# Kernel optimization log

Hardware: AMD Instinct MI355X
Metric: run time of the kernel (lower is better)

Reference implementation:

```python
import jax, jax.numpy as jnp
import numpy as np

BS, SEQ, ML, DEPTH = 32, 50, 16, 4
NN = 2 ** DEPTH - 1          # 15 nodes per complete binary tree (heap layout)
VOCAB, EMB, ENC = 50000, 128, 128
GH = 32                      # bigru hidden per direction
NC = 100                     # num_concepts
LH = 128                     # LSTM hidden
LIN = 2 + 2 * GH + NC + 1    # 167 LSTM feature dim


def _gru_dir(x, Wx, Wh, bx, bh, reverse):
    # x: [B, T, I]; torch GRU gate order r,z,n
    B, H = x.shape[0], Wh.shape[1]
    xe = jnp.einsum('bti,gi->btg', x, Wx) + bx   # [B,T,3H]
    xs = jnp.swapaxes(xe, 0, 1)
    if reverse:
        xs = xs[::-1]
    def step(h, xt):
        gh = h @ Wh.T + bh
        r = jax.nn.sigmoid(xt[:, :H] + gh[:, :H])
        z = jax.nn.sigmoid(xt[:, H:2 * H] + gh[:, H:2 * H])
        n = jnp.tanh(xt[:, 2 * H:] + r * gh[:, 2 * H:])
        hn = (1.0 - z) * n + z * h
        return hn, hn
    _, hs = jax.lax.scan(step, jnp.zeros((B, H), x.dtype), xs)
    if reverse:
        hs = hs[::-1]
    return jnp.swapaxes(hs, 0, 1)


def _lstm(x, Wx, Wh, bx, bh):
    # x: [B, T, I]; torch LSTM gate order i,f,g,o
    B, H = x.shape[0], Wh.shape[1]
    xe = jnp.einsum('bti,gi->btg', x, Wx) + bx   # [B,T,4H]
    def step(carry, xt):
        h, c = carry
        g = xt + h @ Wh.T + bh
        i = jax.nn.sigmoid(g[:, :H])
        f = jax.nn.sigmoid(g[:, H:2 * H])
        gg = jnp.tanh(g[:, 2 * H:3 * H])
        o = jax.nn.sigmoid(g[:, 3 * H:])
        c = f * c + i * gg
        h = o * jnp.tanh(c)
        return (h, c), h
    h0 = (jnp.zeros((B, H), x.dtype), jnp.zeros((B, H), x.dtype))
    _, hs = jax.lax.scan(step, h0, jnp.swapaxes(xe, 0, 1))
    return jnp.swapaxes(hs, 0, 1)


def setup_inputs() -> dict:
    key = jax.random.key(0)
    ks = jax.random.split(key, 24)
    p = {}
    p['p_id'] = jax.random.randint(ks[0], (BS, SEQ), 0, 1000)
    p['c_id'] = jax.random.randint(ks[1], (BS, SEQ), 0, NC)
    p['ast_tokens'] = jax.random.randint(ks[2], (BS, SEQ, ML, NN), 0, VOCAB)
    p['target_c'] = jax.nn.one_hot(jax.random.randint(ks[3], (BS, SEQ), 0, NC + 1), NC + 1, dtype=jnp.float32)
    p['c_embed'] = jax.random.normal(ks[4], (BS, SEQ, NC + 1), jnp.float32)
    p['cur_result'] = jax.random.normal(ks[5], (BS, SEQ, 2), jnp.float32)
    p['result'] = (jax.random.uniform(ks[6], (BS * SEQ,)) < 0.5).astype(jnp.float32)
    p['emb'] = jax.random.normal(ks[7], (VOCAB, EMB), jnp.float32) * 0.02
    p['Wc_w'] = jax.random.normal(ks[8], (ENC, EMB), jnp.float32) / np.sqrt(EMB)
    p['Wc_b'] = jnp.zeros((ENC,), jnp.float32)
    p['gru_WxF'] = jax.random.normal(ks[9], (3 * GH, ENC), jnp.float32) / np.sqrt(ENC)
    p['gru_WhF'] = jax.random.normal(ks[10], (3 * GH, GH), jnp.float32) / np.sqrt(GH)
    p['gru_bxF'] = jnp.zeros((3 * GH,), jnp.float32)
    p['gru_bhF'] = jnp.zeros((3 * GH,), jnp.float32)
    p['gru_WxB'] = jax.random.normal(ks[11], (3 * GH, ENC), jnp.float32) / np.sqrt(ENC)
    p['gru_WhB'] = jax.random.normal(ks[12], (3 * GH, GH), jnp.float32) / np.sqrt(GH)
    p['gru_bxB'] = jnp.zeros((3 * GH,), jnp.float32)
    p['gru_bhB'] = jnp.zeros((3 * GH,), jnp.float32)
    p['lstm_Wx'] = jax.random.normal(ks[13], (4 * LH, LIN), jnp.float32) / np.sqrt(LIN)
    p['lstm_Wh'] = jax.random.normal(ks[14], (4 * LH, LH), jnp.float32) / np.sqrt(LH)
    p['lstm_bx'] = jnp.zeros((4 * LH,), jnp.float32)
    p['lstm_bh'] = jnp.zeros((4 * LH,), jnp.float32)
    p['pred_w'] = jax.random.normal(ks[15], (NC + 1, LH), jnp.float32) / np.sqrt(LH)
    p['pred_b'] = jnp.zeros((NC + 1,), jnp.float32)
    return p


def reference(p_id, c_id, ast_tokens, target_c, c_embed, cur_result, result,
              emb, Wc_w, Wc_b,
              gru_WxF, gru_WhF, gru_bxF, gru_bhF,
              gru_WxB, gru_WhB, gru_bxB, gru_bhB,
              lstm_Wx, lstm_Wh, lstm_bx, lstm_bh,
              pred_w, pred_b):
    # BatchTreeEncoder: per-node W_c(emb(tok)), subtree-sum via bottom-up heap, max over nodes
    e = emb[ast_tokens] @ Wc_w.T + Wc_b          # [BS,SEQ,ML,NN,ENC]
    s = e
    for lvl in range(DEPTH - 2, -1, -1):          # bottom-up over fixed tree levels
        par = np.arange(2 ** lvl - 1, 2 ** (lvl + 1) - 1)
        s = s.at[..., par, :].add(s[..., 2 * par + 1, :] + s[..., 2 * par + 2, :])
    tree_enc = jnp.max(s, axis=3)                 # [BS,SEQ,ML,ENC]
    x = tree_enc.reshape(BS * SEQ, ML, ENC)
    hf = _gru_dir(x, gru_WxF, gru_WhF, gru_bxF, gru_bhF, False)
    hb = _gru_dir(x, gru_WxB, gru_WhB, gru_bxB, gru_bhB, True)
    gout = jnp.concatenate([hf, hb], axis=-1)     # [BS*SEQ, ML, 64]
    code = jnp.max(gout, axis=1).reshape(BS, SEQ, 2 * GH)  # max_pool1d over time
    lin = jnp.concatenate([c_embed, code, cur_result], axis=-1)  # [BS,SEQ,LIN]
    lout = _lstm(lin, lstm_Wx, lstm_Wh, lstm_bx, lstm_bh)         # [BS,SEQ,LH]
    pred = lout.reshape(BS * SEQ, LH) @ pred_w.T + pred_b         # [BS*SEQ, NC+1]
    tc = target_c.reshape(BS * SEQ, NC + 1)
    p1 = jnp.sum(pred * tc, axis=-1)              # bmm(pred, target_c)
    ncon = jnp.sum(tc, axis=-1)
    m = (ncon > 0).astype(pred.dtype)
    fp = p1 / jnp.maximum(ncon, 1.0)
    bce = jnp.maximum(fp, 0.0) - fp * result + jnp.log1p(jnp.exp(-jnp.abs(fp)))
    loss = jnp.sum(bce * m) / jnp.maximum(jnp.sum(m), 1.0)
    return loss, jax.nn.sigmoid(fp) * m, result * m
```

## Files before the change

kernel.cpp:

```cpp
#include <hip/hip_runtime.h>
#include <hip/hip_bf16.h>
#include <math.h>

#define BS 32
#define SEQ 50
#define ML 16
#define NN 15
#define NTREE (BS*SEQ*ML)
#define NROW (BS*SEQ)
#define VOCAB 50000
#define EMB 128
#define ENC 128
#define GH 32
#define NC 100
#define LH 128
#define LIN_D 167

typedef float f32x4 __attribute__((ext_vector_type(4)));
typedef short s16x8 __attribute__((ext_vector_type(8)));
typedef unsigned int u32;
typedef u32 u32x4v __attribute__((ext_vector_type(4)));

#define LOG2E 1.4426950408889634f
__device__ __forceinline__ float fsig(float x) {
  return __builtin_amdgcn_rcpf(1.f + __builtin_amdgcn_exp2f(-LOG2E * x));
}
__device__ __forceinline__ float ftanh(float x) {
  return 2.f * __builtin_amdgcn_rcpf(
             1.f + __builtin_amdgcn_exp2f(-2.f * LOG2E * x)) - 1.f;
}
__device__ __forceinline__ u32 pkbf(float x, float y) {
  u32 a = __float_as_uint(x), b = __float_as_uint(y);
  a = (a + 0x7FFFu + ((a >> 16) & 1u)) >> 16;
  b = (b + 0x7FFFu + ((b >> 16) & 1u)) >> 16;
  return a | (b << 16);
}
__device__ __forceinline__ unsigned short f2bf(float x) {
  u32 a = __float_as_uint(x);
  return (unsigned short)((a + 0x7FFFu + ((a >> 16) & 1u)) >> 16);
}
#define MFMA __builtin_amdgcn_mfma_f32_16x16x32_bf16

__global__ __launch_bounds__(256) void gemm_mfma(
    const float* __restrict__ A, const u32* __restrict__ Bpk,
    const float* __restrict__ bias, void* __restrict__ Cout,
    int M, int N, int out_bf16) {
  int w = threadIdx.x >> 6, lane = threadIdx.x & 63;
  int R0 = blockIdx.x * 64 + w * 16;
  int r = R0 + (lane & 15);
  int rm = (r < M) ? r : (M - 1);
  const float* Ar = A + (size_t)rm * 128 + (lane >> 4) * 8;
  s16x8 a0, a1, a2, a3;
  {
#define LDA(AF, KT) { \
    float4 f0 = *(const float4*)(Ar + KT * 32); \
    float4 f1 = *(const float4*)(Ar + KT * 32 + 4); \
    u32x4v q = {pkbf(f0.x, f0.y), pkbf(f0.z, f0.w), \
                pkbf(f1.x, f1.y), pkbf(f1.z, f1.w)}; \
    AF = __builtin_bit_cast(s16x8, q); }
    LDA(a0, 0) LDA(a1, 1) LDA(a2, 2) LDA(a3, 3)
#undef LDA
  }
  const u32x4v* Bp = (const u32x4v*)Bpk;
  for (int c = 0; c < N; c += 64) {
    f32x4 acc0, acc1, acc2, acc3;
    {
      float b0 = bias ? bias[c + (lane & 15)]      : 0.f;
      float b1 = bias ? bias[c + 16 + (lane & 15)] : 0.f;
      float b2 = bias ? bias[c + 32 + (lane & 15)] : 0.f;
      float b3 = bias ? bias[c + 48 + (lane & 15)] : 0.f;
      acc0 = (f32x4){b0, b0, b0, b0}; acc1 = (f32x4){b1, b1, b1, b1};
      acc2 = (f32x4){b2, b2, b2, b2}; acc3 = (f32x4){b3, b3, b3, b3};
    }
    int fbase = (c >> 4) * 4;
#define DONT(ACC, NT) { \
    s16x8 bf0 = __builtin_bit_cast(s16x8, Bp[(size_t)(fbase + NT * 4 + 0) * 64 + lane]); \
    s16x8 bf1 = __builtin_bit_cast(s16x8, Bp[(size_t)(fbase + NT * 4 + 1) * 64 + lane]); \
    s16x8 bf2 = __builtin_bit_cast(s16x8, Bp[(size_t)(fbase + NT * 4 + 2) * 64 + lane]); \
    s16x8 bf3 = __builtin_bit_cast(s16x8, Bp[(size_t)(fbase + NT * 4 + 3) * 64 + lane]); \
    ACC = MFMA(a0, bf0, ACC, 0, 0, 0); ACC = MFMA(a1, bf1, ACC, 0, 0, 0); \
    ACC = MFMA(a2, bf2, ACC, 0, 0, 0); ACC = MFMA(a3, bf3, ACC, 0, 0, 0); }
    DONT(acc0, 0) DONT(acc1, 1) DONT(acc2, 2) DONT(acc3, 3)
#undef DONT
    int colb = c + (lane & 15);
    int rowb = R0 + (lane >> 4) * 4;
#define STNT(ACC, NT) \
    _Pragma("unroll") \
    for (int j = 0; j < 4; j++) { \
      int row = rowb + j; \
      if (row < M) { \
        if (out_bf16) ((unsigned short*)Cout)[(size_t)row * N + colb + NT * 16] = f2bf(ACC[j]); \
        else ((float*)Cout)[(size_t)row * N + colb + NT * 16] = ACC[j]; \
      } \
    }
    STNT(acc0, 0) STNT(acc1, 1) STNT(acc2, 2) STNT(acc3, 3)
#undef STNT
  }
}

__global__ __launch_bounds__(256) void gemm_mfma_bfA(
    const unsigned short* __restrict__ Ab, const u32* __restrict__ Bpk,
    const float* __restrict__ bias, float* __restrict__ Cout,
    int M, int N) {
  int w = threadIdx.x >> 6, lane = threadIdx.x & 63;
  int R0 = blockIdx.x * 64 + w * 16;
  int r = R0 + (lane & 15);
  int rm = (r < M) ? r : (M - 1);
  const unsigned short* Ar = Ab + (size_t)rm * 128 + (lane >> 4) * 8;
  s16x8 a0 = *(const s16x8*)(Ar + 0);
  s16x8 a1 = *(const s16x8*)(Ar + 32);
  s16x8 a2 = *(const s16x8*)(Ar + 64);
  s16x8 a3 = *(const s16x8*)(Ar + 96);
  const u32x4v* Bp = (const u32x4v*)Bpk;
  for (int c = 0; c < N; c += 64) {
    f32x4 acc0, acc1, acc2, acc3;
    {
      float b0 = bias[c + (lane & 15)];
      float b1 = bias[c + 16 + (lane & 15)];
      float b2 = bias[c + 32 + (lane & 15)];
      float b3 = bias[c + 48 + (lane & 15)];
      acc0 = (f32x4){b0, b0, b0, b0}; acc1 = (f32x4){b1, b1, b1, b1};
      acc2 = (f32x4){b2, b2, b2, b2}; acc3 = (f32x4){b3, b3, b3, b3};
    }
    int fbase = (c >> 4) * 4;
#define DONT(ACC, NT) { \
    s16x8 bf0 = __builtin_bit_cast(s16x8, Bp[(size_t)(fbase + NT * 4 + 0) * 64 + lane]); \
    s16x8 bf1 = __builtin_bit_cast(s16x8, Bp[(size_t)(fbase + NT * 4 + 1) * 64 + lane]); \
    s16x8 bf2 = __builtin_bit_cast(s16x8, Bp[(size_t)(fbase + NT * 4 + 2) * 64 + lane]); \
    s16x8 bf3 = __builtin_bit_cast(s16x8, Bp[(size_t)(fbase + NT * 4 + 3) * 64 + lane]); \
    ACC = MFMA(a0, bf0, ACC, 0, 0, 0); ACC = MFMA(a1, bf1, ACC, 0, 0, 0); \
    ACC = MFMA(a2, bf2, ACC, 0, 0, 0); ACC = MFMA(a3, bf3, ACC, 0, 0, 0); }
    DONT(acc0, 0) DONT(acc1, 1) DONT(acc2, 2) DONT(acc3, 3)
#undef DONT
    int colb = c + (lane & 15);
    int rowb = R0 + (lane >> 4) * 4;
#define STNT(ACC, NT) \
    _Pragma("unroll") \
    for (int j = 0; j < 4; j++) { \
      int row = rowb + j; \
      if (row < M) Cout[(size_t)row * N + colb + NT * 16] = ACC[j]; \
    }
    STNT(acc0, 0) STNT(acc1, 1) STNT(acc2, 2) STNT(acc3, 3)
#undef STNT
  }
}

__device__ __forceinline__ float lin_at(const float* __restrict__ ce,
    const float* __restrict__ co, const float* __restrict__ cu,
    int row, int k) {
  if (k < 101) return ce[row * 101 + k];
  if (k < 165) return co[row * 64 + (k - 101)];
  if (k < 167) return cu[row * 2 + (k - 165)];
  return 0.f;
}

__global__ __launch_bounds__(256) void gemm_lin(
    const float* __restrict__ c_embed, const float* __restrict__ code,
    const float* __restrict__ cur, const u32* __restrict__ Bpk,
    const float* __restrict__ bias, float* __restrict__ Cout) {
  int w = threadIdx.x >> 6, lane = threadIdx.x & 63;
  int R0 = blockIdx.x * 64 + w * 16;
  int r = R0 + (lane & 15);
  s16x8 a[6];
  #pragma unroll
  for (int kt = 0; kt < 6; kt++) {
    int k0 = kt * 32 + (lane >> 4) * 8;
    float f[8];
    #pragma unroll
    for (int j = 0; j < 8; j++) f[j] = lin_at(c_embed, code, cur, r, k0 + j);
    u32x4v q = {pkbf(f[0], f[1]), pkbf(f[2], f[3]),
                pkbf(f[4], f[5]), pkbf(f[6], f[7])};
    a[kt] = __builtin_bit_cast(s16x8, q);
  }
  const u32x4v* Bp = (const u32x4v*)Bpk;
  for (int c = 0; c < 512; c += 64) {
    f32x4 acc[4];
    #pragma unroll
    for (int nt = 0; nt < 4; nt++) {
      float bv = bias[c + nt * 16 + (lane & 15)];
      acc[nt] = (f32x4){bv, bv, bv, bv};
    }
    int fbase = (c >> 4) * 6;
    #pragma unroll
    for (int nt = 0; nt < 4; nt++) {
      #pragma unroll
      for (int kt = 0; kt < 6; kt++) {
        s16x8 bf = __builtin_bit_cast(s16x8,
            Bp[(size_t)(fbase + nt * 6 + kt) * 64 + lane]);
        acc[nt] = MFMA(a[kt], bf, acc[nt], 0, 0, 0);
      }
    }
    int colb = c + (lane & 15);
    int rowb = R0 + (lane >> 4) * 4;
    #pragma unroll
    for (int nt = 0; nt < 4; nt++)
      #pragma unroll
      for (int j = 0; j < 4; j++)
        Cout[(size_t)(rowb + j) * 512 + colb + nt * 16] = acc[nt][j];
  }
}

__global__ __launch_bounds__(256) void k_prep(const float* __restrict__ WxF,
    const float* __restrict__ WxB, const float* __restrict__ bxF,
    const float* __restrict__ bxB, const float* __restrict__ lstm_Wx,
    const float* __restrict__ lstm_Wh, const float* __restrict__ Wc_w,
    const float* __restrict__ gru_WhF, const float* __restrict__ gru_WhB,
    float* __restrict__ ball, u32* __restrict__ Wcpk,
    u32* __restrict__ Wallpk, u32* __restrict__ Wxpk, u32* __restrict__ Wpk,
    u32* __restrict__ Wgpk) {
  int i = blockIdx.x * 256 + threadIdx.x;
  if (i < 96) ball[i] = bxF[i];
  else if (i < 192) ball[i] = bxB[i - 96];
  if (i < 8192) {
    int fg = i >> 8, l = (i >> 2) & 63, p = i & 3;
    int nt = fg >> 2, kt = fg & 3;
    int n = nt * 16 + (l & 15);
    int k = kt * 32 + (l >> 4) * 8 + 2 * p;
    Wcpk[i] = pkbf(Wc_w[n * 128 + k], Wc_w[n * 128 + k + 1]);
  }
  if (i < 12288) {
    int fg = i >> 8, l = (i >> 2) & 63, p = i & 3;
    int nt = fg >> 2, kt = fg & 3;
    int n = nt * 16 + (l & 15);
    int k = kt * 32 + (l >> 4) * 8 + 2 * p;
    float v0 = (n < 96) ? WxF[n * 128 + k]     : WxB[(n - 96) * 128 + k];
    float v1 = (n < 96) ? WxF[n * 128 + k + 1] : WxB[(n - 96) * 128 + k + 1];
    Wallpk[i] = pkbf(v0, v1);
  }
  if (i < 49152) {
    int fg = i >> 8, l = (i >> 2) & 63, p = i & 3;
    int nt = fg / 6, kt = fg % 6;
    int n = nt * 16 + (l & 15);
    int k = kt * 32 + (l >> 4) * 8 + 2 * p;
    float v0 = (k < LIN_D)     ? lstm_Wx[n * LIN_D + k]     : 0.f;
    float v1 = (k + 1 < LIN_D) ? lstm_Wx[n * LIN_D + k + 1] : 0.f;
    Wxpk[i] = pkbf(v0, v1);
  }
  if (i < 32768) {
    int fg = i >> 8, l = (i >> 2) & 63, p = i & 3;
    int w = fg >> 4, gt = (fg >> 2) & 3, kt = fg & 3;
    int n = 128 * gt + 16 * w + (l & 15);
    int k = 32 * kt + 8 * (l >> 4) + 2 * p;
    Wpk[i] = pkbf(lstm_Wh[n * 128 + k], lstm_Wh[n * 128 + k + 1]);
  }
  if (i < 3072) {
    int fg = i >> 8, l = (i >> 2) & 63, p = i & 3;
    int dir = fg / 6, nt = fg % 6;
    int n = nt * 16 + (l & 15);
    int k = (l >> 4) * 8 + 2 * p;
    const float* Wh = dir ? gru_WhB : gru_WhF;
    Wgpk[i] = pkbf(Wh[n * 32 + k], Wh[n * 32 + k + 1]);
  }
}

__global__ __launch_bounds__(256) void k_tree(const int* __restrict__ ast,
    const u32* __restrict__ Epb, const float* __restrict__ Wc_b,
    unsigned short* __restrict__ x_bf) {
  int lt = threadIdx.x >> 7;
  int d  = threadIdx.x & 127;
  int tree = blockIdx.x * 2 + lt;
  __shared__ int toks[2][15];
  if (d < 15) toks[lt][d] = ast[(size_t)tree * 15 + d];
  __syncthreads();
  float e[15];
  int half = d >> 1;
  bool odd = (d & 1) != 0;
  #pragma unroll
  for (int n = 0; n < 15; n++) {
    u32 v = Epb[(size_t)toks[lt][n] * 64 + half];
    e[n] = __uint_as_float(odd ? (v & 0xFFFF0000u) : (v << 16));
  }
  float b = Wc_b[d];
  float s3 = e[3] + e[7] + e[8],  s4 = e[4] + e[9] + e[10];
  float s5 = e[5] + e[11] + e[12], s6 = e[6] + e[13] + e[14];
  float s1 = e[1] + s3 + s4, s2 = e[2] + s5 + s6;
  float s0 = e[0] + s1 + s2;
  float ml = fmaxf(fmaxf(fmaxf(e[7], e[8]), fmaxf(e[9], e[10])),
                   fmaxf(fmaxf(e[11], e[12]), fmaxf(e[13], e[14]))) + b;
  float mm = fmaxf(fmaxf(s3, s4), fmaxf(s5, s6)) + 3.f * b;
  float mt = fmaxf(s1, s2) + 7.f * b;
  float m = fmaxf(fmaxf(ml, mm), fmaxf(mt, s0 + 15.f * b));
  x_bf[(size_t)tree * 128 + d] = f2bf(m);
}

__global__ __launch_bounds__(256) void k_gru(const float* __restrict__ xe_all,
    const u32* __restrict__ Wgpk, const float* __restrict__ bhF,
    const float* __restrict__ bhB, float* __restrict__ code) {
  __shared__ float xls[32 * 192];
  __shared__ short hls[4][32];
  int t = threadIdx.x, w = t >> 6, lane = t & 63;
  int sq0 = blockIdx.x * 2;
  const float* xb = xe_all + (size_t)sq0 * 16 * 192;
  #pragma unroll 4
  for (int i = t; i < 32 * 192; i += 256) xls[i] = xb[i];
  int sql = w >> 1, dir = w & 1;
  int seq = sq0 + sql;
  const s16x8* BG = (const s16x8*)Wgpk + (size_t)dir * 6 * 64 + lane;
  s16x8 G0 = BG[0], G1 = BG[64], G2 = BG[128];
  s16x8 G3 = BG[192], G4 = BG[256], G5 = BG[320];
  const float* bh = dir ? bhB : bhF;
  float bh0 = 0, bh1 = 0, bh2 = 0, bh3 = 0, bh4 = 0, bh5 = 0;
  if (lane < 16) {
    bh0 = bh[lane];      bh1 = bh[16 + lane]; bh2 = bh[32 + lane];
    bh3 = bh[48 + lane]; bh4 = bh[64 + lane]; bh5 = bh[80 + lane];
  }
  float h0 = 0.f, h1 = 0.f, mx0 = -1e30f, mx1 = -1e30f;
  hls[w][lane & 31] = 0;
  __syncthreads();
  const s16x8 zz = {0, 0, 0, 0, 0, 0, 0, 0};
  const bool arow = (lane & 15) == 0;
  const int aoff = (lane >> 4) * 8;
  for (int s = 0; s < 16; s++) {
    int tt = dir ? (15 - s) : s;
    const float* xr = xls + (sql * 16 + tt) * 192 + dir * 96;
    s16x8 a = arow ? *(const s16x8*)&hls[w][aoff] : zz;
    f32x4 ac0 = {0,0,0,0}, ac1 = {0,0,0,0}, ac2 = {0,0,0,0};
    f32x4 ac3 = {0,0,0,0}, ac4 = {0,0,0,0}, ac5 = {0,0,0,0};
    float xn0 = 0.f, xn1 = 0.f;
    if (lane < 16) {
      ac0[0] = xr[lane] + bh0;      ac1[0] = xr[16 + lane] + bh1;
      ac2[0] = xr[32 + lane] + bh2; ac3[0] = xr[48 + lane] + bh3;
      ac4[0] = bh4;                 ac5[0] = bh5;
      xn0 = xr[64 + lane];          xn1 = xr[80 + lane];
    }
    ac0 = MFMA(a, G0, ac0, 0, 0, 0); ac1 = MFMA(a, G1, ac1, 0, 0, 0);
    ac2 = MFMA(a, G2, ac2, 0, 0, 0); ac3 = MFMA(a, G3, ac3, 0, 0, 0);
    ac4 = MFMA(a, G4, ac4, 0, 0, 0); ac5 = MFMA(a, G5, ac5, 0, 0, 0);
    if (lane < 16) {
      float r0 = fsig(ac0[0]), r1 = fsig(ac1[0]);
      float z0 = fsig(ac2[0]), z1 = fsig(ac3[0]);
      float n0 = ftanh(xn0 + r0 * ac4[0]);
      float n1 = ftanh(xn1 + r1 * ac5[0]);
      h0 = (1.f - z0) * n0 + z0 * h0;
      h1 = (1.f - z1) * n1 + z1 * h1;
      mx0 = fmaxf(mx0, h0); mx1 = fmaxf(mx1, h1);
      hls[w][lane]      = (short)f2bf(h0);
      hls[w][16 + lane] = (short)f2bf(h1);
    }
  }
  if (lane < 16) {
    code[(size_t)seq * 64 + dir * 32 + lane]      = mx0;
    code[(size_t)seq * 64 + dir * 32 + 16 + lane] = mx1;
  }
}

__global__ __launch_bounds__(512) void k_lstm(
    const float* __restrict__ xeL, const u32* __restrict__ Wpk,
    const float* __restrict__ bh, float* __restrict__ lout) {
  __shared__ float xl[SEQ * 512];
  __shared__ float hh[SEQ * 128];
  __shared__ s16x8 hl8[16];
  short* hls = (short*)hl8;
  int b = blockIdx.x, t = threadIdx.x;
  int w = t >> 6, lane = t & 63;
  const float* xrow = xeL + (size_t)b * SEQ * 512;
  #pragma unroll 5
  for (int i = t; i < SEQ * 512; i += 512) xl[i] = xrow[i];
  const s16x8* WB = (const s16x8*)Wpk + (size_t)w * 16 * 64 + lane;
  s16x8 B00 = WB[0*64],  B01 = WB[1*64],  B02 = WB[2*64],  B03 = WB[3*64];
  s16x8 B10 = WB[4*64],  B11 = WB[5*64],  B12 = WB[6*64],  B13 = WB[7*64];
  s16x8 B20 = WB[8*64],  B21 = WB[9*64],  B22 = WB[10*64], B23 = WB[11*64];
  s16x8 B30 = WB[12*64], B31 = WB[13*64], B32 = WB[14*64], B33 = WB[15*64];

  int u16 = 16 * w + lane;
  float bh0 = 0, bh1 = 0, bh2 = 0, bh3 = 0;
  if (lane < 16) {
    bh0 = bh[u16]; bh1 = bh[128 + u16]; bh2 = bh[256 + u16]; bh3 = bh[384 + u16];
  }
  float c = 0.f;
  if (t < 128) hls[t] = 0;
  __syncthreads();
  const s16x8 zz = {0, 0, 0, 0, 0, 0, 0, 0};
  const bool arow = (lane & 15) == 0;
  const int asel = lane >> 4;
  for (int step = 0; step < SEQ; step++) {
    s16x8 a0 = arow ? hl8[asel]      : zz;
    s16x8 a1 = arow ? hl8[4 + asel]  : zz;
    s16x8 a2 = arow ? hl8[8 + asel]  : zz;
    s16x8 a3 = arow ? hl8[12 + asel] : zz;
    f32x4 acc0 = {0, 0, 0, 0}, acc1 = {0, 0, 0, 0};
    f32x4 acc2 = {0, 0, 0, 0}, acc3 = {0, 0, 0, 0};
    if (lane < 16) {
      const float* xs = xl + step * 512;
      acc0[0] = xs[u16]       + bh0;
      acc1[0] = xs[128 + u16] + bh1;
      acc2[0] = xs[256 + u16] + bh2;
      acc3[0] = xs[384 + u16] + bh3;
    }
    acc0 = MFMA(a0, B00, acc0, 0, 0, 0); acc0 = MFMA(a1, B01, acc0, 0, 0, 0);
    acc0 = MFMA(a2, B02, acc0, 0, 0, 0); acc0 = MFMA(a3, B03, acc0, 0, 0, 0);
    acc1 = MFMA(a0, B10, acc1, 0, 0, 0); acc1 = MFMA(a1, B11, acc1, 0, 0, 0);
    acc1 = MFMA(a2, B12, acc1, 0, 0, 0); acc1 = MFMA(a3, B13, acc1, 0, 0, 0);
    acc2 = MFMA(a0, B20, acc2, 0, 0, 0); acc2 = MFMA(a1, B21, acc2, 0, 0, 0);
    acc2 = MFMA(a2, B22, acc2, 0, 0, 0); acc2 = MFMA(a3, B23, acc2, 0, 0, 0);
    acc3 = MFMA(a0, B30, acc3, 0, 0, 0); acc3 = MFMA(a1, B31, acc3, 0, 0, 0);
    acc3 = MFMA(a2, B32, acc3, 0, 0, 0); acc3 = MFMA(a3, B33, acc3, 0, 0, 0);
    if (lane < 16) {
      float iv = fsig(acc0[0]);
      float fv = fsig(acc1[0]);
      float gv = ftanh(acc2[0]);
      float ov = fsig(acc3[0]);
      c = fv * c + iv * gv;
      float h = ov * ftanh(c);
      hh[step * 128 + u16] = h;
      hls[u16] = (short)f2bf(h);
    }
    __syncthreads();
  }
  float* lo = lout + (size_t)b * SEQ * 128;
  #pragma unroll 4
  for (int i = t; i < SEQ * 128; i += 512) lo[i] = hh[i];
}

__global__ __launch_bounds__(128) void k_pred(const float* __restrict__ lout,
    const float* __restrict__ pred_w, const float* __restrict__ pred_b,
    const float* __restrict__ tc, const float* __restrict__ result,
    float* __restrict__ out, float* __restrict__ fpbuf, float* __restrict__ mbuf) {
  int row = blockIdx.x; int k = threadIdx.x;
  __shared__ float tcs[101];
  __shared__ float r1[128], r2[128], r3[128];
  if (k < 101) tcs[k] = tc[(size_t)row * 101 + k];
  __syncthreads();
  float nz = 0.f, ixs = 0.f, vs = 0.f;
  if (k < 101 && tcs[k] != 0.f) { nz = 1.f; ixs = (float)k; vs = tcs[k]; }
  r1[k] = nz; r2[k] = ixs; r3[k] = vs;
  __syncthreads();
  for (int st = 64; st > 0; st >>= 1) {
    if (k < st) { r1[k] += r1[k + st]; r2[k] += r2[k + st]; r3[k] += r3[k + st]; }
    __syncthreads();
  }
  float cnt = r1[0], idxf = r2[0], ncon = r3[0];
  __syncthreads();
  float fp, m;
  if (cnt == 1.f && ncon == 1.f) {
    int cls = (int)idxf;
    float v = lout[(size_t)row * 128 + k] * pred_w[cls * 128 + k];
    r1[k] = v;
    __syncthreads();
    for (int st = 64; st > 0; st >>= 1) {
      if (k < st) r1[k] += r1[k + st];
      __syncthreads();
    }
    fp = r1[0] + pred_b[cls];
    m = 1.f;
  } else {
    float lk = lout[(size_t)row * 128 + k];
    float acc = 0.f;
    for (int c = 0; c < 101; c++) acc += tcs[c] * pred_w[c * 128 + k];
    float v = acc * lk;
    float pb = (k < 101) ? tcs[k] * pred_b[k] : 0.f;
    r1[k] = v; r2[k] = pb;
    __syncthreads();
    for (int st = 64; st > 0; st >>= 1) {
      if (k < st) { r1[k] += r1[k + st]; r2[k] += r2[k + st]; }
      __syncthreads();
    }
    m = (ncon > 0.f) ? 1.f : 0.f;
    fp = (r1[0] + r2[0]) / fmaxf(ncon, 1.f);
  }
  if (k == 0) {
    fpbuf[row] = fp; mbuf[row] = m;
    out[1 + row] = m / (1.f + expf(-fp));
    out[1 + NROW + row] = result[row] * m;
  }
}

__global__ __launch_bounds__(256) void k_loss(const float* __restrict__ fpbuf,
    const float* __restrict__ mbuf, const float* __restrict__ result,
    float* __restrict__ out) {
  __shared__ float sb[256], sm[256];
  int k = threadIdx.x;
  float ab = 0.f, am = 0.f;
  for (int r = k; r < NROW; r += 256) {
    float fp = fpbuf[r], m = mbuf[r], res = result[r];
    float bce = fmaxf(fp, 0.f) - fp * res + log1pf(expf(-fabsf(fp)));
    ab += bce * m; am += m;
  }
  sb[k] = ab; sm[k] = am;
  __syncthreads();
  for (int st = 128; st > 0; st >>= 1) {
    if (k < st) { sb[k] += sb[k + st]; sm[k] += sm[k + st]; }
    __syncthreads();
  }
  if (k == 0) out[0] = sb[0] / fmaxf(sm[0], 1.f);
}

extern "C" void kernel_launch(void* const* d_in, const int* in_sizes, int n_in,
                              void* d_out, int out_size, void* d_ws, size_t ws_size,
                              hipStream_t stream) {
  (void)in_sizes; (void)n_in; (void)out_size; (void)ws_size;
  const int*   ast      = (const int*)  d_in[2];
  const float* target_c = (const float*)d_in[3];
  const float* c_embed  = (const float*)d_in[4];
  const float* cur_res  = (const float*)d_in[5];
  const float* result   = (const float*)d_in[6];
  const float* emb      = (const float*)d_in[7];
  const float* Wc_w     = (const float*)d_in[8];
  const float* Wc_b     = (const float*)d_in[9];
  const float* gru_WxF  = (const float*)d_in[10];
  const float* gru_WhF  = (const float*)d_in[11];
  const float* gru_bxF  = (const float*)d_in[12];
  const float* gru_bhF  = (const float*)d_in[13];
  const float* gru_WxB  = (const float*)d_in[14];
  const float* gru_WhB  = (const float*)d_in[15];
  const float* gru_bxB  = (const float*)d_in[16];
  const float* gru_bhB  = (const float*)d_in[17];
  const float* lstm_Wx  = (const float*)d_in[18];
  const float* lstm_Wh  = (const float*)d_in[19];
  const float* lstm_bx  = (const float*)d_in[20];
  const float* lstm_bh  = (const float*)d_in[21];
  const float* pred_w   = (const float*)d_in[22];
  const float* pred_b   = (const float*)d_in[23];
  float* out = (float*)d_out;

  float* W = (float*)d_ws;
  u32*   Epb    = (u32*)W;
  unsigned short* x_bf = (unsigned short*)(W + 3200000);
  float* xe_all = W + 4838400;
  float* code   = W + 9753600;
  float* xeL    = W + 9856000;
  float* lout   = W + 10675200;
  float* fpbuf  = W + 10880000;
  float* mbuf   = W + 10881600;
  u32*   Wcpk   = (u32*)(W + 10883200);
  u32*   Wallpk = (u32*)(W + 10891392);
  u32*   Wxpk   = (u32*)(W + 10903680);
  u32*   Wpk    = (u32*)(W + 10952832);
  float* ball   = W + 10985600;
  u32*   Wgpk   = (u32*)(W + 10985792);

  k_prep<<<192, 256, 0, stream>>>(gru_WxF, gru_WxB, gru_bxF, gru_bxB, lstm_Wx,
                                  lstm_Wh, Wc_w, gru_WhF, gru_WhB,
                                  ball, Wcpk, Wallpk, Wxpk, Wpk, Wgpk);
  gemm_mfma<<<782, 256, 0, stream>>>(emb, Wcpk, nullptr, Epb, VOCAB, 128, 1);
  k_tree<<<NTREE / 2, 256, 0, stream>>>(ast, Epb, Wc_b, x_bf);
  gemm_mfma_bfA<<<400, 256, 0, stream>>>(x_bf, Wallpk, ball, xe_all, NTREE, 192);
  k_gru<<<NROW / 2, 256, 0, stream>>>(xe_all, Wgpk, gru_bhF, gru_bhB, code);
  gemm_lin<<<25, 256, 0, stream>>>(c_embed, code, cur_res, Wxpk, lstm_bx, xeL);
  k_lstm<<<BS, 512, 0, stream>>>(xeL, Wpk, lstm_bh, lout);
  k_pred<<<NROW, 128, 0, stream>>>(lout, pred_w, pred_b, target_c, result,
                                   out, fpbuf, mbuf);
  k_loss<<<1, 256, 0, stream>>>(fpbuf, mbuf, result, out);
}
```

Baseline: 133.2 us.

## Fuse tree encoder into GRU input-projection GEMM, building A fragments in registers

Merges the tree-encoding kernel into the bf16 MFMA GEMM. Each lane gathers the embedding rows for its tree and builds its MFMA A-operand fragments directly in registers, so the intermediate x_bf buffer is never written or read back. This also saves one kernel launch. In exchange, the fused kernel runs only 400 blocks, where the old tree kernel ran 12800. Each lane also holds 15 gathered 16-byte vectors, which raises register pressure and may leave less parallelism to hide the gather latency.

```diff
diff --git a/kernel.cpp b/kernel.cpp
--- a/kernel.cpp
+++ b/kernel.cpp
@@ -98,21 +98,56 @@
   }
 }
 
-__global__ __launch_bounds__(256) void gemm_mfma_bfA(
-    const unsigned short* __restrict__ Ab, const u32* __restrict__ Bpk,
-    const float* __restrict__ bias, float* __restrict__ Cout,
-    int M, int N) {
-  int w = threadIdx.x >> 6, lane = threadIdx.x & 63;
-  int R0 = blockIdx.x * 64 + w * 16;
-  int r = R0 + (lane & 15);
-  int rm = (r < M) ? r : (M - 1);
-  const unsigned short* Ar = Ab + (size_t)rm * 128 + (lane >> 4) * 8;
-  s16x8 a0 = *(const s16x8*)(Ar + 0);
-  s16x8 a1 = *(const s16x8*)(Ar + 32);
-  s16x8 a2 = *(const s16x8*)(Ar + 64);
-  s16x8 a3 = *(const s16x8*)(Ar + 96);
+__global__ __launch_bounds__(256) void k_tree_xe(
+    const int* __restrict__ ast, const u32* __restrict__ Epb,
+    const float* __restrict__ Wc_b, const u32* __restrict__ Bpk,
+    const float* __restrict__ bias, float* __restrict__ Cout) {
+  __shared__ int toks[64 * 15];
+  int t = threadIdx.x, w = t >> 6, lane = t & 63;
+  int R0 = blockIdx.x * 64;
+  const int* ab = ast + (size_t)R0 * 15;
+  #pragma unroll
+  for (int i = t; i < 960; i += 256) toks[i] = ab[i];
+  __syncthreads();
+  int rl = w * 16 + (lane & 15);
+  int q = lane >> 4;
+  const u32x4v* Epg = (const u32x4v*)Epb;
+  s16x8 afr0, afr1, afr2, afr3;
+#define BUILD(AF, KT) { \
+    u32x4v g[15]; \
+    _Pragma("unroll") \
+    for (int n = 0; n < 15; n++) \
+      g[n] = Epg[(size_t)toks[rl * 15 + n] * 16 + KT * 4 + q]; \
+    u32 outw[4]; \
+    _Pragma("unroll") \
+    for (int j = 0; j < 4; j++) { \
+      float m2[2]; \
+      _Pragma("unroll") \
+      for (int hilo = 0; hilo < 2; hilo++) { \
+        float e[15]; \
+        _Pragma("unroll") \
+        for (int n = 0; n < 15; n++) \
+          e[n] = __uint_as_float(hilo ? (g[n][j] & 0xFFFF0000u) : (g[n][j] << 16)); \
+        float b = Wc_b[KT * 32 + q * 8 + 2 * j + hilo]; \
+        float s3 = e[3] + e[7] + e[8],  s4 = e[4] + e[9] + e[10]; \
+        float s5 = e[5] + e[11] + e[12], s6 = e[6] + e[13] + e[14]; \
+        float s1 = e[1] + s3 + s4, s2 = e[2] + s5 + s6; \
+        float s0 = e[0] + s1 + s2; \
+        float ml = fmaxf(fmaxf(fmaxf(e[7], e[8]), fmaxf(e[9], e[10])), \
+                         fmaxf(fmaxf(e[11], e[12]), fmaxf(e[13], e[14]))) + b; \
+        float mm = fmaxf(fmaxf(s3, s4), fmaxf(s5, s6)) + 3.f * b; \
+        float mt = fmaxf(s1, s2) + 7.f * b; \
+        m2[hilo] = fmaxf(fmaxf(ml, mm), fmaxf(mt, s0 + 15.f * b)); \
+      } \
+      outw[j] = pkbf(m2[0], m2[1]); \
+    } \
+    u32x4v qq = {outw[0], outw[1], outw[2], outw[3]}; \
+    AF = __builtin_bit_cast(s16x8, qq); }
+  BUILD(afr0, 0) BUILD(afr1, 1) BUILD(afr2, 2) BUILD(afr3, 3)
+#undef BUILD
   const u32x4v* Bp = (const u32x4v*)Bpk;
-  for (int c = 0; c < N; c += 64) {
+  int R0w = R0 + w * 16;
+  for (int c = 0; c < 192; c += 64) {
     f32x4 acc0, acc1, acc2, acc3;
     {
       float b0 = bias[c + (lane & 15)];
@@ -128,18 +163,16 @@
     s16x8 bf1 = __builtin_bit_cast(s16x8, Bp[(size_t)(fbase + NT * 4 + 1) * 64 + lane]); \
     s16x8 bf2 = __builtin_bit_cast(s16x8, Bp[(size_t)(fbase + NT * 4 + 2) * 64 + lane]); \
     s16x8 bf3 = __builtin_bit_cast(s16x8, Bp[(size_t)(fbase + NT * 4 + 3) * 64 + lane]); \
-    ACC = MFMA(a0, bf0, ACC, 0, 0, 0); ACC = MFMA(a1, bf1, ACC, 0, 0, 0); \
-    ACC = MFMA(a2, bf2, ACC, 0, 0, 0); ACC = MFMA(a3, bf3, ACC, 0, 0, 0); }
+    ACC = MFMA(afr0, bf0, ACC, 0, 0, 0); ACC = MFMA(afr1, bf1, ACC, 0, 0, 0); \
+    ACC = MFMA(afr2, bf2, ACC, 0, 0, 0); ACC = MFMA(afr3, bf3, ACC, 0, 0, 0); }
     DONT(acc0, 0) DONT(acc1, 1) DONT(acc2, 2) DONT(acc3, 3)
 #undef DONT
     int colb = c + (lane & 15);
-    int rowb = R0 + (lane >> 4) * 4;
+    int rowb = R0w + (lane >> 4) * 4;
 #define STNT(ACC, NT) \
     _Pragma("unroll") \
-    for (int j = 0; j < 4; j++) { \
-      int row = rowb + j; \
-      if (row < M) Cout[(size_t)row * N + colb + NT * 16] = ACC[j]; \
-    }
+    for (int j = 0; j < 4; j++) \
+      Cout[(size_t)(rowb + j) * 192 + colb + NT * 16] = ACC[j];
     STNT(acc0, 0) STNT(acc1, 1) STNT(acc2, 2) STNT(acc3, 3)
 #undef STNT
   }
@@ -251,36 +284,6 @@
     const float* Wh = dir ? gru_WhB : gru_WhF;
     Wgpk[i] = pkbf(Wh[n * 32 + k], Wh[n * 32 + k + 1]);
   }
-}
-
-__global__ __launch_bounds__(256) void k_tree(const int* __restrict__ ast,
-    const u32* __restrict__ Epb, const float* __restrict__ Wc_b,
-    unsigned short* __restrict__ x_bf) {
-  int lt = threadIdx.x >> 7;
-  int d  = threadIdx.x & 127;
-  int tree = blockIdx.x * 2 + lt;
-  __shared__ int toks[2][15];
-  if (d < 15) toks[lt][d] = ast[(size_t)tree * 15 + d];
-  __syncthreads();
-  float e[15];
-  int half = d >> 1;
-  bool odd = (d & 1) != 0;
-  #pragma unroll
-  for (int n = 0; n < 15; n++) {
-    u32 v = Epb[(size_t)toks[lt][n] * 64 + half];
-    e[n] = __uint_as_float(odd ? (v & 0xFFFF0000u) : (v << 16));
-  }
-  float b = Wc_b[d];
-  float s3 = e[3] + e[7] + e[8],  s4 = e[4] + e[9] + e[10];
-  float s5 = e[5] + e[11] + e[12], s6 = e[6] + e[13] + e[14];
-  float s1 = e[1] + s3 + s4, s2 = e[2] + s5 + s6;
-  float s0 = e[0] + s1 + s2;
-  float ml = fmaxf(fmaxf(fmaxf(e[7], e[8]), fmaxf(e[9], e[10])),
-                   fmaxf(fmaxf(e[11], e[12]), fmaxf(e[13], e[14]))) + b;
-  float mm = fmaxf(fmaxf(s3, s4), fmaxf(s5, s6)) + 3.f * b;
-  float mt = fmaxf(s1, s2) + 7.f * b;
-  float m = fmaxf(fmaxf(ml, mm), fmaxf(mt, s0 + 15.f * b));
-  x_bf[(size_t)tree * 128 + d] = f2bf(m);
 }
 
 __global__ __launch_bounds__(256) void k_gru(const float* __restrict__ xe_all,
@@ -515,26 +518,24 @@
 
   float* W = (float*)d_ws;
   u32*   Epb    = (u32*)W;
-  unsigned short* x_bf = (unsigned short*)(W + 3200000);
-  float* xe_all = W + 4838400;
-  float* code   = W + 9753600;
-  float* xeL    = W + 9856000;
-  float* lout   = W + 10675200;
-  float* fpbuf  = W + 10880000;
-  float* mbuf   = W + 10881600;
-  u32*   Wcpk   = (u32*)(W + 10883200);
-  u32*   Wallpk = (u32*)(W + 10891392);
-  u32*   Wxpk   = (u32*)(W + 10903680);
-  u32*   Wpk    = (u32*)(W + 10952832);
-  float* ball   = W + 10985600;
-  u32*   Wgpk   = (u32*)(W + 10985792);
+  float* xe_all = W + 3200000;
+  float* code   = W + 8115200;
+  float* xeL    = W + 8217600;
+  float* lout   = W + 9036800;
+  float* fpbuf  = W + 9241600;
+  float* mbuf   = W + 9243200;
+  u32*   Wcpk   = (u32*)(W + 9244800);
+  u32*   Wallpk = (u32*)(W + 9252992);
+  u32*   Wxpk   = (u32*)(W + 9265280);
+  u32*   Wpk    = (u32*)(W + 9314432);
+  float* ball   = W + 9347200;
+  u32*   Wgpk   = (u32*)(W + 9347392);
 
   k_prep<<<192, 256, 0, stream>>>(gru_WxF, gru_WxB, gru_bxF, gru_bxB, lstm_Wx,
                                   lstm_Wh, Wc_w, gru_WhF, gru_WhB,
                                   ball, Wcpk, Wallpk, Wxpk, Wpk, Wgpk);
   gemm_mfma<<<782, 256, 0, stream>>>(emb, Wcpk, nullptr, Epb, VOCAB, 128, 1);
-  k_tree<<<NTREE / 2, 256, 0, stream>>>(ast, Epb, Wc_b, x_bf);
-  gemm_mfma_bfA<<<400, 256, 0, stream>>>(x_bf, Wallpk, ball, xe_all, NTREE, 192);
+  k_tree_xe<<<400, 256, 0, stream>>>(ast, Epb, Wc_b, Wallpk, ball, xe_all);
   k_gru<<<NROW / 2, 256, 0, stream>>>(xe_all, Wgpk, gru_bhF, gru_bhB, code);
   gemm_lin<<<25, 256, 0, stream>>>(c_embed, code, cur_res, Wxpk, lstm_bx, xeL);
   k_lstm<<<BS, 512, 0, stream>>>(xeL, Wpk, lstm_bh, lout);
```

Measured after the change: 134.1 us. Within noise of the previous version (+0.7%).
